# Performance work log

Hardware: AMD Instinct MI355X
Metric: run time of the kernel (lower is better)

## Reference

```python
import jax, jax.numpy as jnp
import numpy as np

B, S, D, DOM, L = 16, 512, 512, 8, 3  # batch, seq_len, mem_dim (S==D required by outputs*rel), domains, layers


def setup_inputs() -> dict:
    key = jax.random.key(0)
    ks = jax.random.split(key, 16)
    adj = jax.random.uniform(ks[0], (B, S, S), jnp.float32)
    rel = jax.random.uniform(ks[1], (B, S, S), jnp.float32)
    gcn_inputs = jax.random.normal(ks[2], (B, S, D), jnp.float32)
    frontrel = jax.random.normal(ks[3], (B, S, D), jnp.float32)
    backrel = jax.random.normal(ks[4], (B, S, D), jnp.float32)
    # depmap: exactly one selected column per (b, row) so masked_select reshapes to [B,S]
    depmap = jax.nn.one_hot(jax.random.randint(ks[5], (B, S), 0, S), S, dtype=jnp.float32)
    dom_idx = jax.random.randint(ks[6], (B, S), 0, DOM)
    has_dom = jax.random.bernoulli(ks[7], 0.5, (B, S)).astype(jnp.float32)
    domain_id = jax.nn.one_hot(dom_idx, DOM, dtype=jnp.float32) * has_dom[..., None]
    redom_idx = jax.random.randint(ks[8], (B, S), 0, DOM)
    has_re = jax.random.bernoulli(ks[9], 0.5, (B, S)).astype(jnp.float32)
    redomain_id = jax.nn.one_hot(redom_idx, DOM, dtype=jnp.float32) * has_re[..., None]
    domain = jax.random.bernoulli(ks[10], 0.5, (B, S, DOM, 1))
    mask = jnp.ones((B, S), dtype=bool)
    sc = 1.0 / np.sqrt(D)
    W_layers = jax.random.normal(ks[11], (L, D, D), jnp.float32) * sc
    b_layers = jnp.zeros((L, D), jnp.float32)
    prelu_a = jnp.full((L,), 0.25, jnp.float32)  # nn.PReLU default
    W_dg = jax.random.normal(ks[12], (D, D), jnp.float32) * sc
    b_dg = jnp.zeros((D,), jnp.float32)
    W_mg = jax.random.normal(ks[13], (2 * D, D), jnp.float32) * (1.0 / np.sqrt(2 * D))
    b_mg = jnp.zeros((D,), jnp.float32)
    W_out = jax.random.normal(ks[14], (L * D, D), jnp.float32) * (1.0 / np.sqrt(L * D))
    b_out = jnp.zeros((D,), jnp.float32)
    return dict(adj=adj, domain=domain, domain_id=domain_id, redomain_id=redomain_id,
                frontrel=frontrel, backrel=backrel, depmap=depmap, rel=rel,
                gcn_inputs=gcn_inputs, mask=mask, W_layers=W_layers, b_layers=b_layers,
                prelu_a=prelu_a, W_dg=W_dg, b_dg=b_dg, W_mg=W_mg, b_mg=b_mg,
                W_out=W_out, b_out=b_out)


def _forward(adj, domain, domain_id, redomain_id, frontrel, backrel, depmap, rel,
             gcn_inputs, W_layers, b_layers, prelu_a, W_dg, b_dg, W_mg, b_mg, W_out, b_out):
    denom = jnp.sum(adj, axis=2, keepdims=True) + 1.0                     # [B,S,1]
    domain_mask = jnp.sum(domain_id, axis=-1, keepdims=True) == 1.0       # [B,S,1]
    redomain_mask = jnp.sum(redomain_id, axis=-1, keepdims=True) == 1.0   # [B,S,1]
    frontadj = jnp.sum(adj * depmap, axis=-1)                             # [B,S]
    backadj = jnp.sum(jnp.swapaxes(adj, -1, -2) * depmap, axis=-1)        # [B,S]
    outputs = gcn_inputs
    outs = []
    for l in range(L):
        frontoutputs = jnp.where(domain_mask, 0.0, outputs)
        backoutputs = jnp.where(redomain_mask, 0.0, jnp.einsum('bij,bjd->bid', rel, outputs))
        # domain pooling: mask then max over sequence -> [B,DOM,D]
        pooled = jnp.max(jnp.where(domain, -10000.0, outputs[:, :, None, :]), axis=1)
        domain_outputs = jax.nn.sigmoid(pooled @ W_dg + b_dg)             # domain_gate
        frontoutputs = frontoutputs + jnp.einsum('bsk,bkd->bsd', domain_id, domain_outputs)
        backoutputs = backoutputs + jnp.einsum('bsk,bkd->bsd', redomain_id, domain_outputs)
        frontdepadj = jax.nn.sigmoid(jnp.concatenate([frontoutputs, frontrel], -1) @ W_mg + b_mg)
        backdepadj = jax.nn.sigmoid(jnp.concatenate([backoutputs, backrel], -1) @ W_mg + b_mg)
        delta = jnp.einsum('bji,bjd->bid', rel, frontadj[..., None] * frontdepadj * frontoutputs)
        delta = delta + backadj[..., None] * backdepadj * backoutputs
        Ax = jnp.einsum('bij,bjd->bid', adj, outputs * rel)               # requires S==D
        AxW = (Ax @ W_layers[l] + b_layers[l]) + (outputs @ W_layers[l] + b_layers[l]) + delta
        x = AxW / denom
        outputs = jnp.where(x >= 0, x, prelu_a[l] * x)                    # PReLU
        outs.append(outputs)                                              # dropout is eval-mode identity
    gcn_outputs = jnp.concatenate(outs, axis=2)                           # [B,S,L*D]
    return gcn_outputs @ W_out + b_out + gcn_inputs


def reference(adj, domain, domain_id, redomain_id, frontrel, backrel, depmap, rel,
              gcn_inputs, mask, W_layers, b_layers, prelu_a, W_dg, b_dg, W_mg, b_mg,
              W_out, b_out):
    return _forward(adj, domain, domain_id, redomain_id, frontrel, backrel, depmap, rel,
                    gcn_inputs, W_layers, b_layers, prelu_a, W_dg, b_dg, W_mg, b_mg,
                    W_out, b_out)
```

## Files before the change

### kernel.cpp

```cpp
#include <hip/hip_runtime.h>
#include <math.h>

#define SD_  (512*512)
#define BSD_ (16*512*512)

typedef unsigned short u16;
typedef short s16x8 __attribute__((ext_vector_type(8)));
typedef float f32x4 __attribute__((ext_vector_type(4)));

__device__ __forceinline__ float sigmoidf_(float x) { return 1.0f / (1.0f + __expf(-x)); }

__device__ __forceinline__ u16 f2bf(float f) {
    unsigned int u = __float_as_uint(f);
    u += 0x7fffu + ((u >> 16) & 1u);
    return (u16)(u >> 16);
}
__device__ __forceinline__ float bf2f(u16 h) { return __uint_as_float((unsigned)h << 16); }

__device__ __forceinline__ void glds16(const void* g, void* l) {
    __builtin_amdgcn_global_load_lds((const __attribute__((address_space(1))) unsigned int*)g,
                                     (__attribute__((address_space(3))) unsigned int*)l, 16, 0, 0);
}

struct GP {
    const u16 *A1, *A2;  int lda1, lda2;  long sA;
    const u16 *B1, *B2;  int ldb1, ldb2;  long sB;
    void *C1, *C2;  int obf1, obf2, ldc1, ldc2;  long sC;
    u16 *CT1, *CT2;  long sCT;
    const void *Ci1, *Ci2;  int cm1, cm2, ldci1, ldci2;  long sCi1, sCi2;
    const float *bias;  float bS;
    const float *sc1, *sc2;
    const int *selm1, *seli1, *selm2, *seli2;
    const float *DG;
    const float *invden, *prelu;  int pidx;
    int M, K, zs, swzX, swzY;
};

template<int EPI, int ASEL>
__global__ __launch_bounds__(512, 4)
void gemm3(const GP p)
{
    __shared__ short LS[32768];
    const int tid = threadIdx.x;
    int bx, by, bz;
    if (p.swzX >= 0) {
        const int bid = blockIdx.x + gridDim.x * (blockIdx.y + gridDim.y * blockIdx.z);
        const int ppx = (gridDim.y * gridDim.z) >> 3;
        const int xcd = bid & 7, idx = bid >> 3;
        const int pair = xcd * ppx + (idx >> p.swzX);
        bx = idx & ((1 << p.swzX) - 1);
        by = pair & ((1 << p.swzY) - 1);
        bz = pair >> p.swzY;
    } else { bx = blockIdx.x; by = blockIdx.y; bz = blockIdx.z; }

    const int seg = (bz >= p.zs) ? 1 : 0;
    const int z = seg ? bz - p.zs : bz;
    const u16* Ab = (seg ? p.A2 : p.A1) + z * p.sA;
    const int lda = seg ? p.lda2 : p.lda1;
    const u16* Bb = (seg ? p.B2 : p.B1) + z * p.sB;
    const int ldb = seg ? p.ldb2 : p.ldb1;

    const int m0 = by * 128, n0 = bx * 128;
    const int srow = ((tid >> 6) << 4) | (tid & 15);
    const int sk0 = ((tid >> 4) & 3) << 3;

    const u16* aRow = Ab + (long)(m0 + srow) * lda + sk0;
    const u16* bRow = Bb + (long)(n0 + srow) * ldb + sk0;

    int aselv = 0; long dgo = 0;
    if (ASEL) {
        const int* selm = seg ? p.selm2 : p.selm1;
        const int* seli = seg ? p.seli2 : p.seli1;
        const int r0 = m0 + srow;
        aselv = selm[r0];
        dgo = (long)(((r0 >> 9) << 3) + seli[r0]) * 512 + sk0;
    }

    auto stage = [&](int kk, int buf) {
        short* base = &LS[buf * 8192];
        if (ASEL) {
            s16x8 v;
            if (aselv) {
                const float* dg = p.DG + dgo + kk;
#pragma unroll
                for (int q = 0; q < 8; ++q) v[q] = (short)f2bf(dg[q]);
            } else v = *(const s16x8*)(aRow + kk);
            *(s16x8*)&base[tid * 8] = v;
        } else {
            glds16(aRow + kk, &base[tid * 8]);
        }
        glds16(bRow + kk, &base[4096 + tid * 8]);
    };

    const int wave = tid >> 6, lane = tid & 63;
    const int gA = (wave >> 2) << 2;
    const int gB = (wave & 3) << 1;

    f32x4 acc[4][2] = {};
    const int nkb = p.K >> 5;
    stage(0, 0);
    stage(32, 1);
    for (int kb = 0; kb < nkb; ++kb) {
        if (kb + 2 < nkb) stage((kb + 2) << 5, (kb + 2) & 3);
        const int ahead = (nkb - 1 - kb) < 2 ? (nkb - 1 - kb) : 2;
        if (ASEL) {
            if (ahead == 2)      asm volatile("s_waitcnt vmcnt(2)" ::: "memory");
            else if (ahead == 1) asm volatile("s_waitcnt vmcnt(1)" ::: "memory");
            else                 asm volatile("s_waitcnt vmcnt(0)" ::: "memory");
            asm volatile("s_waitcnt lgkmcnt(0)" ::: "memory");
        } else {
            if (ahead == 2)      asm volatile("s_waitcnt vmcnt(4)" ::: "memory");
            else if (ahead == 1) asm volatile("s_waitcnt vmcnt(2)" ::: "memory");
            else                 asm volatile("s_waitcnt vmcnt(0)" ::: "memory");
        }
        __builtin_amdgcn_s_barrier();
        const short* ls = &LS[(kb & 3) * 8192];
        s16x8 aF[4], bF[2];
#pragma unroll
        for (int mt = 0; mt < 4; ++mt) aF[mt] = *(const s16x8*)&ls[((gA + mt) * 64 + lane) * 8];
#pragma unroll
        for (int nt = 0; nt < 2; ++nt) bF[nt] = *(const s16x8*)&ls[4096 + ((gB + nt) * 64 + lane) * 8];
#pragma unroll
        for (int mt = 0; mt < 4; ++mt)
#pragma unroll
            for (int nt = 0; nt < 2; ++nt)
                acc[mt][nt] = __builtin_amdgcn_mfma_f32_16x16x32_bf16(aF[mt], bF[nt], acc[mt][nt], 0, 0, 0);
    }

    const int ml = lane & 15, quad = lane >> 4;
    const int wm = (wave >> 2) * 64, wn = (wave & 3) * 32;
    u16* Cb16 = (u16*)(seg ? p.C2 : p.C1);
    float* Cb32 = (float*)(seg ? p.C2 : p.C1);
    const int haveC = (seg ? p.C2 : p.C1) != nullptr;
    const int obf = seg ? p.obf2 : p.obf1;
    const int ldc = seg ? p.ldc2 : p.ldc1;
    if (haveC) { if (obf) Cb16 += z * p.sC; else Cb32 += z * p.sC; }
    u16* CTb = seg ? p.CT2 : p.CT1;
    if (CTb) CTb += z * p.sCT;
    const u16* CiT = (const u16*)(seg ? p.Ci2 : p.Ci1);
    const float* Ci32 = (const float*)(seg ? p.Ci2 : p.Ci1);
    const int cm = seg ? p.cm2 : p.cm1;
    const int ldci = seg ? p.ldci2 : p.ldci1;
    {
        const long sCi = seg ? p.sCi2 : p.sCi1;
        if (cm) CiT += z * sCi; else Ci32 += z * sCi;
    }
    const float pal = (EPI == 4) ? p.prelu[p.pidx] : 0.0f;
    const float* scp = (EPI == 8) ? (seg ? p.sc2 : p.sc1) : nullptr;
    const int* eselm = (EPI == 8) ? (seg ? p.selm2 : p.selm1) : nullptr;
    const int* eseli = (EPI == 8) ? (seg ? p.selm2 ? (seg ? p.seli2 : p.seli1) : p.seli1 : p.seli1) : nullptr;
    const int* eseli2 = (EPI == 8) ? (seg ? p.seli2 : p.seli1) : nullptr;

    const bool useEp = haveC && (obf == 1);
    u16* epbuf = (u16*)LS;
    if (useEp) __syncthreads();

#pragma unroll
    for (int mt = 0; mt < 4; ++mt) {
#pragma unroll
        for (int nt = 0; nt < 2; ++nt) {
            const int col = n0 + wn + nt * 16 + ml;
            const int rowb = m0 + wm + mt * 16 + quad * 4;
            float cin4[4];
            if (EPI == 3 || EPI == 4 || EPI == 7 || EPI == 8) {
                if (cm) {
                    const ushort4 c4 = *(const ushort4*)&CiT[(long)(rowb >> 9) * SD_ + (long)col * 512 + (rowb & 511)];
                    cin4[0] = bf2f(c4.x); cin4[1] = bf2f(c4.y); cin4[2] = bf2f(c4.z); cin4[3] = bf2f(c4.w);
                } else {
#pragma unroll
                    for (int r = 0; r < 4; ++r) cin4[r] = Ci32[(long)(rowb + r) * ldci + col];
                }
            }
            u16 pk[4];
#pragma unroll
            for (int r = 0; r < 4; ++r) {
                const int row = rowb + r;
                float x = acc[mt][nt][r];
                if (EPI == 1) x += p.bias[col];
                else if (EPI == 3) x += cin4[r];
                else if (EPI == 4) {
                    x = (x + p.bS * p.bias[col] + cin4[r]) * p.invden[z * p.M + row];
                    x = (x >= 0.0f) ? x : pal * x;
                }
                else if (EPI == 6) x = sigmoidf_(x + p.bias[col]);
                else if (EPI == 7) x += p.bias[col] + cin4[r];
                else if (EPI == 8) {
                    float av;
                    if (eselm[row]) av = p.DG[(long)(((row >> 9) << 3) + eseli2[row]) * 512 + col];
                    else av = bf2f(Ab[(long)row * lda + col]);
                    x = sigmoidf_(x + cin4[r]) * scp[row] * av;
                }
                if (haveC && obf == 0) Cb32[(long)row * ldc + col] = x;
                pk[r] = f2bf(x);
                if (useEp) epbuf[(wm + mt * 16 + quad * 4 + r) * 136 + wn + nt * 16 + ml] = pk[r];
            }
            if (CTb) {
                u16* ct = CTb + (long)(rowb >> 9) * SD_ + (long)col * 512 + (rowb & 511);
                *(ushort4*)ct = *(ushort4*)pk;
            }
        }
    }
    if (useEp) {
        __syncthreads();
        const int lr = tid >> 2, cs = (tid & 3) * 32;
#pragma unroll
        for (int j = 0; j < 4; ++j) {
            const s16x8 v = *(const s16x8*)&epbuf[lr * 136 + cs + j * 8];
            *(s16x8*)&Cb16[(long)(m0 + lr) * ldc + n0 + cs + j * 8] = v;
        }
    }
}

__global__ __launch_bounds__(256)
void cvt_k(const float* __restrict__ s, u16* __restrict__ d)
{
    const long i = ((long)blockIdx.x * 256 + threadIdx.x) * 4;
    const float4 v = *(const float4*)&s[i];
    ushort4 h = { f2bf(v.x), f2bf(v.y), f2bf(v.z), f2bf(v.w) };
    *(ushort4*)&d[i] = h;
}

__global__ __launch_bounds__(256)
void trcvt_k(const float* __restrict__ src, u16* __restrict__ dstT, u16* __restrict__ dstN,
             const int R, const int C, const long sS, const long sDT, const long sDN)
{
    __shared__ u16 t[64][72];
    const float* s = src + blockIdx.z * sS;
    const int r0 = blockIdx.y * 64, c0 = blockIdx.x * 64;
    const int tid = threadIdx.x;
    const int lr = tid >> 2, lc4 = (tid & 3) * 16;
#pragma unroll
    for (int j = 0; j < 4; ++j) {
        const float4 v = *(const float4*)&s[(long)(r0 + lr) * C + c0 + lc4 + j * 4];
        ushort4 h = { f2bf(v.x), f2bf(v.y), f2bf(v.z), f2bf(v.w) };
        *(ushort4*)&t[lr][lc4 + j * 4] = h;
        if (dstN) *(ushort4*)&dstN[blockIdx.z * sDN + (long)(r0 + lr) * C + c0 + lc4 + j * 4] = h;
    }
    __syncthreads();
    const int lcol = tid >> 2, rc = (tid & 3) * 16;
#pragma unroll
    for (int j = 0; j < 2; ++j) {
        s16x8 v;
#pragma unroll
        for (int q = 0; q < 8; ++q) v[q] = (short)t[rc + j * 8 + q][lcol];
        *(s16x8*)&dstT[blockIdx.z * sDT + (long)(c0 + lcol) * R + r0 + rc + j * 8] = v;
    }
}

__global__ __launch_bounds__(256)
void e0_k(const float* __restrict__ adj, const float* __restrict__ depmap,
          const float* __restrict__ domain_id, const float* __restrict__ redomain_id,
          float* __restrict__ invden, float* __restrict__ fa, int* __restrict__ dcol,
          int* __restrict__ dm, int* __restrict__ dsel, int* __restrict__ rm, int* __restrict__ rsel)
{
    const int bs = blockIdx.x;
    const int t = threadIdx.x;
    const float* arow = adj + (long)bs * 512;
    const float* drow = depmap + (long)bs * 512;
    __shared__ float red[256];
    __shared__ int scol;
    if (t == 0) scol = 0;
    const float a0 = arow[t], a1 = arow[t + 256];
    const float p0 = drow[t], p1 = drow[t + 256];
    if (p0 > 0.5f) scol = t;
    if (p1 > 0.5f) scol = t + 256;
    red[t] = a0 + a1;
    __syncthreads();
    for (int off = 128; off > 0; off >>= 1) { if (t < off) red[t] += red[t + off]; __syncthreads(); }
    if (t == 0) invden[bs] = 1.0f / (red[0] + 1.0f);
    __syncthreads();
    red[t] = a0 * p0 + a1 * p1;
    __syncthreads();
    for (int off = 128; off > 0; off >>= 1) { if (t < off) red[t] += red[t + off]; __syncthreads(); }
    if (t == 0) {
        fa[bs] = red[0];
        dcol[bs] = scol;
        const float* q = domain_id + (long)bs * 8;
        float s = 0.f; int sel = 0;
        for (int k = 0; k < 8; ++k) { float v = q[k]; s += v; if (v > 0.5f) sel = k; }
        dm[bs] = (s > 0.5f) ? 1 : 0; dsel[bs] = sel;
        const float* r = redomain_id + (long)bs * 8;
        s = 0.f; sel = 0;
        for (int k = 0; k < 8; ++k) { float v = r[k]; s += v; if (v > 0.5f) sel = k; }
        rm[bs] = (s > 0.5f) ? 1 : 0; rsel[bs] = sel;
    }
}

__global__ void e0b_k(const float* __restrict__ adj, const int* __restrict__ dcol, float* __restrict__ ba)
{
    const int bs = blockIdx.x * 256 + threadIdx.x;
    const int b = bs >> 9, s = bs & 511;
    ba[bs] = adj[((long)b * 512 + dcol[bs]) * 512 + s];
}

__global__ __launch_bounds__(256)
void pool1_k(const u16* __restrict__ OUT, const int ldO, const int* __restrict__ domain,
             const u16* __restrict__ relb, u16* __restrict__ cm, u16* __restrict__ OxRT)
{
    const int b = blockIdx.x >> 4, c = blockIdx.x & 15;
    const int s0 = c * 32, tid = threadIdx.x;
    __shared__ int dom[256];
    dom[tid] = domain[((long)(b * 512 + s0 + (tid >> 3))) * 8 + (tid & 7)];
    __syncthreads();
    const int d0 = tid * 2;
    float mxa[8], mxb[8];
#pragma unroll
    for (int k = 0; k < 8; ++k) { mxa[k] = -10000.0f; mxb[k] = -10000.0f; }
    s16x8 pA[4], pB[4];
#pragma unroll
    for (int s = 0; s < 32; ++s) {
        const int row = b * 512 + s0 + s;
        const unsigned uv = *(const unsigned*)&OUT[(long)row * ldO + d0];
        const unsigned rv = *(const unsigned*)&relb[(long)row * 512 + d0];
        const float vx = bf2f((u16)(uv & 0xffff)), vy = bf2f((u16)(uv >> 16));
        const float rx = bf2f((u16)(rv & 0xffff)), ry = bf2f((u16)(rv >> 16));
        pA[s >> 3][s & 7] = (short)f2bf(vx * rx);
        pB[s >> 3][s & 7] = (short)f2bf(vy * ry);
        const int* ds = &dom[s * 8];
#pragma unroll
        for (int k = 0; k < 8; ++k) {
            mxa[k] = fmaxf(mxa[k], ds[k] ? -10000.0f : vx);
            mxb[k] = fmaxf(mxb[k], ds[k] ? -10000.0f : vy);
        }
    }
#pragma unroll
    for (int j = 0; j < 4; ++j) *(s16x8*)&OxRT[((long)b * 512 + d0) * 512 + s0 + j * 8] = pA[j];
#pragma unroll
    for (int j = 0; j < 4; ++j) *(s16x8*)&OxRT[((long)b * 512 + d0 + 1) * 512 + s0 + j * 8] = pB[j];
#pragma unroll
    for (int k = 0; k < 8; ++k) {
        ushort2 h = { f2bf(mxa[k]), f2bf(mxb[k]) };
        *(ushort2*)&cm[((long)((b * 16 + c) * 8 + k)) * 512 + d0] = h;
    }
}

__global__ void pool2_k(const u16* __restrict__ cm, u16* __restrict__ pooled)
{
    const int q = blockIdx.x * 256 + threadIdx.x;
    const int b = q >> 12, k = (q >> 9) & 7, d = q & 511;
    float m = -1e30f;
    for (int c = 0; c < 16; ++c)
        m = fmaxf(m, bf2f(cm[((long)((b * 16 + c) * 8 + k)) * 512 + d]));
    pooled[((long)(b * 8 + k)) * 512 + d] = f2bf(m);
}

extern "C" void kernel_launch(void* const* d_in, const int* in_sizes, int n_in,
                              void* d_out, int out_size, void* d_ws, size_t ws_size,
                              hipStream_t stream)
{
    const float* adj         = (const float*)d_in[0];
    const int*   domain      = (const int*)d_in[1];
    const float* domain_id   = (const float*)d_in[2];
    const float* redomain_id = (const float*)d_in[3];
    const float* frontrel    = (const float*)d_in[4];
    const float* backrel     = (const float*)d_in[5];
    const float* depmap      = (const float*)d_in[6];
    const float* rel         = (const float*)d_in[7];
    const float* gcn         = (const float*)d_in[8];
    const float* W_layers    = (const float*)d_in[10];
    const float* b_layers    = (const float*)d_in[11];
    const float* prelu_a     = (const float*)d_in[12];
    const float* W_dg        = (const float*)d_in[13];
    const float* b_dg        = (const float*)d_in[14];
    const float* W_mg        = (const float*)d_in[15];
    const float* b_mg        = (const float*)d_in[16];
    const float* W_out       = (const float*)d_in[17];
    const float* b_out       = (const float*)d_in[18];
    float* out = (float*)d_out;

    char* w = (char*)d_ws;
    auto alloc = [&](size_t bytes) { void* p = (void*)w; w += (bytes + 255) & ~(size_t)255; return p; };
    const size_t Bb = (size_t)BSD_ * 2;
    u16* OUTS_bf = (u16*)alloc((size_t)8192 * 1536 * 2);
    u16* OUTT    = (u16*)alloc(Bb);
    u16* gcnT    = (u16*)alloc(Bb);
    u16* RB_bf   = (u16*)alloc(Bb);
    u16* XBT     = (u16*)alloc(Bb);
    u16* XFT     = (u16*)alloc(Bb);
    u16* OxRT    = (u16*)alloc(Bb);
    u16* DLT     = (u16*)alloc(Bb);
    u16* AXO_bf  = (u16*)alloc(Bb);
    u16* BBT     = (u16*)alloc(Bb);
    u16* FBT     = (u16*)alloc(Bb);
    u16* rel_bf  = (u16*)alloc(Bb);
    u16* relT_bf = (u16*)alloc(Bb);
    u16* adj_bf  = (u16*)alloc(Bb);
    u16* gcn_bf  = (u16*)alloc(Bb);
    u16* frel_bf = (u16*)alloc(Bb);
    u16* brel_bf = (u16*)alloc(Bb);
    u16* WmgT1 = (u16*)alloc((size_t)SD_ * 2);
    u16* WmgT2 = (u16*)alloc((size_t)SD_ * 2);
    u16* WdgT  = (u16*)alloc((size_t)SD_ * 2);
    u16* WlT   = (u16*)alloc((size_t)3 * SD_ * 2);
    u16* WoutT = (u16*)alloc((size_t)512 * 1536 * 2);
    u16* cm     = (u16*)alloc((size_t)16 * 16 * 8 * 512 * 2);
    u16* pooled = (u16*)alloc((size_t)16 * 8 * 512 * 2);
    float* DG     = (float*)alloc((size_t)16 * 8 * 512 * 4);
    float* invden = (float*)alloc(8192 * 4);
    float* fa     = (float*)alloc(8192 * 4);
    float* ba     = (float*)alloc(8192 * 4);
    int* dcol = (int*)alloc(8192 * 4);
    int* dm   = (int*)alloc(8192 * 4);
    int* dsel = (int*)alloc(8192 * 4);
    int* rm   = (int*)alloc(8192 * 4);
    int* rsel = (int*)alloc(8192 * 4);

    cvt_k<<<4096, 256, 0, stream>>>(adj, adj_bf);
    cvt_k<<<4096, 256, 0, stream>>>(frontrel, frel_bf);
    cvt_k<<<4096, 256, 0, stream>>>(backrel, brel_bf);
    trcvt_k<<<dim3(8, 8, 16), 256, 0, stream>>>(gcn, gcnT, gcn_bf, 512, 512, SD_, SD_, SD_);
    trcvt_k<<<dim3(8, 8, 16), 256, 0, stream>>>(rel, relT_bf, rel_bf, 512, 512, SD_, SD_, SD_);
    trcvt_k<<<dim3(8, 8, 1), 256, 0, stream>>>(W_mg, WmgT1, nullptr, 512, 512, 0, 0, 0);
    trcvt_k<<<dim3(8, 8, 1), 256, 0, stream>>>(W_mg + SD_, WmgT2, nullptr, 512, 512, 0, 0, 0);
    trcvt_k<<<dim3(8, 8, 1), 256, 0, stream>>>(W_dg, WdgT, nullptr, 512, 512, 0, 0, 0);
    trcvt_k<<<dim3(8, 8, 3), 256, 0, stream>>>(W_layers, WlT, nullptr, 512, 512, SD_, SD_, 0);
    trcvt_k<<<dim3(8, 24, 1), 256, 0, stream>>>(W_out, WoutT, nullptr, 1536, 512, 0, 0, 0);
    e0_k<<<8192, 256, 0, stream>>>(adj, depmap, domain_id, redomain_id, invden, fa, dcol, dm, dsel, rm, rsel);
    e0b_k<<<32, 256, 0, stream>>>(adj, dcol, ba);

    const dim3 blk(512);

    {
        GP p{};
        p.A1 = brel_bf; p.A2 = frel_bf; p.lda1 = p.lda2 = 512; p.sA = 0;
        p.B1 = p.B2 = WmgT2; p.ldb1 = p.ldb2 = 512; p.sB = 0;
        p.CT1 = BBT; p.CT2 = FBT; p.sCT = 0;
        p.bias = b_mg; p.M = 8192; p.K = 512; p.zs = 1; p.swzX = 2; p.swzY = 6;
        gemm3<1, 0><<<dim3(4, 64, 2), blk, 0, stream>>>(p);
    }

    for (int l = 0; l < 3; ++l) {
        const u16* OUTp  = (l == 0) ? gcn_bf : (OUTS_bf + (l - 1) * 512);
        const u16* OUTTp = (l == 0) ? gcnT : OUTT;
        const int ldO = (l == 0) ? 512 : 1536;

        {
            GP p{};
            p.A1 = rel_bf; p.lda1 = 512; p.sA = SD_;
            p.B1 = OUTTp; p.ldb1 = 512; p.sB = SD_;
            p.C1 = RB_bf; p.obf1 = 1; p.ldc1 = 512; p.sC = SD_;
            p.M = 512; p.K = 512; p.zs = 16; p.swzX = 2; p.swzY = 2;
            gemm3<0, 0><<<dim3(4, 4, 16), blk, 0, stream>>>(p);
        }
        pool1_k<<<256, 256, 0, stream>>>(OUTp, ldO, domain, rel_bf, cm, OxRT);
        pool2_k<<<256, 256, 0, stream>>>(cm, pooled);
        {
            GP p{};
            p.A1 = pooled; p.lda1 = 512; p.B1 = WdgT; p.ldb1 = 512;
            p.C1 = DG; p.obf1 = 0; p.ldc1 = 512;
            p.bias = b_dg; p.M = 128; p.K = 512; p.zs = 1; p.swzX = -1;
            gemm3<6, 0><<<dim3(4, 1, 1), blk, 0, stream>>>(p);
        }
        {
            GP p{};
            p.A1 = RB_bf; p.lda1 = 512; p.A2 = OUTp; p.lda2 = ldO; p.sA = 0;
            p.selm1 = rm; p.seli1 = rsel; p.selm2 = dm; p.seli2 = dsel; p.DG = DG;
            p.B1 = p.B2 = WmgT1; p.ldb1 = p.ldb2 = 512; p.sB = 0;
            p.Ci1 = BBT; p.Ci2 = FBT; p.cm1 = p.cm2 = 1; p.ldci1 = p.ldci2 = 512; p.sCi1 = p.sCi2 = 0;
            p.CT1 = XBT; p.CT2 = XFT; p.sCT = 0;
            p.sc1 = ba; p.sc2 = fa; p.M = 8192; p.K = 512; p.zs = 1; p.swzX = 2; p.swzY = 6;
            gemm3<8, 1><<<dim3(4, 64, 2), blk, 0, stream>>>(p);
        }
        {
            GP p{};
            p.A1 = relT_bf; p.lda1 = 512; p.A2 = adj_bf; p.lda2 = 512; p.sA = SD_;
            p.B1 = XFT; p.ldb1 = 512;
            p.B2 = OxRT; p.ldb2 = 512; p.sB = SD_;
            p.Ci1 = XBT; p.cm1 = 1; p.ldci1 = 512; p.sCi1 = SD_;
            p.Ci2 = OUTTp; p.cm2 = 1; p.ldci2 = 512; p.sCi2 = SD_;
            p.CT1 = DLT; p.sCT = SD_;
            p.C2 = AXO_bf; p.obf2 = 1; p.ldc2 = 512; p.sC = SD_;
            p.M = 512; p.K = 512; p.zs = 16; p.swzX = 2; p.swzY = 2;
            gemm3<3, 0><<<dim3(4, 4, 32), blk, 0, stream>>>(p);
        }
        {
            GP p{};
            p.A1 = AXO_bf; p.lda1 = 512; p.sA = SD_;
            p.B1 = WlT + (long)l * SD_; p.ldb1 = 512; p.sB = 0;
            p.Ci1 = DLT; p.cm1 = 1; p.ldci1 = 512; p.sCi1 = SD_;
            p.C1 = OUTS_bf + l * 512; p.obf1 = 1; p.ldc1 = 1536; p.sC = (long)512 * 1536;
            p.CT1 = OUTT; p.sCT = SD_;
            p.bias = b_layers + l * 512; p.bS = 2.0f;
            p.invden = invden; p.prelu = prelu_a; p.pidx = l;
            p.M = 512; p.K = 512; p.zs = 16; p.swzX = 2; p.swzY = 2;
            gemm3<4, 0><<<dim3(4, 4, 16), blk, 0, stream>>>(p);
        }
    }

    {
        GP p{};
        p.A1 = OUTS_bf; p.lda1 = 1536; p.sA = 0;
        p.B1 = WoutT; p.ldb1 = 1536; p.sB = 0;
        p.Ci1 = gcn; p.cm1 = 0; p.ldci1 = 512; p.sCi1 = 0;
        p.C1 = out; p.obf1 = 0; p.ldc1 = 512; p.sC = 0;
        p.bias = b_out; p.M = 8192; p.K = 1536; p.zs = 1; p.swzX = 2; p.swzY = 6;
        gemm3<7, 0><<<dim3(4, 64, 1), blk, 0, stream>>>(p);
    }
}
```

Before: 756.7 us.

## Use BK=64 double-buffered async LDS staging and bf16 DG for selected rows

The GEMM main loop now stages 64-wide K tiles into two LDS buffers and issues four global_load_lds per tile, replacing the previous triple-buffered 32-wide scheme. The DG gate matrix is now written and read as bf16. This lets ASEL rows also use async direct-to-LDS loads by redirecting the row pointer, instead of register loads that convert fp32 to bf16. The aim is fewer barriers and waitcnt stalls per K and no per-element conversion in staging, at the cost of an extra barrier per iteration, a shallower prefetch depth and rounding DG to bf16 in the epilogue.

```diff
diff --git a/kernel.cpp b/kernel.cpp
--- a/kernel.cpp
+++ b/kernel.cpp
@@ -31,7 +31,7 @@
     const float *bias;  float bS;
     const float *sc1, *sc2;
     const int *selm1, *seli1, *selm2, *seli2;
-    const float *DG;
+    const u16 *DG;
     const float *invden, *prelu;  int pidx;
     int M, K, zs, swzX, swzY;
 };
@@ -63,33 +63,24 @@
     const int m0 = by * 128, n0 = bx * 128;
     const int srow = ((tid >> 6) << 4) | (tid & 15);
     const int sk0 = ((tid >> 4) & 3) << 3;
+    const int slot = ((srow >> 4) << 9) + (sk0 << 4) + ((srow & 15) << 3);
 
     const u16* aRow = Ab + (long)(m0 + srow) * lda + sk0;
-    const u16* bRow = Bb + (long)(n0 + srow) * ldb + sk0;
-
-    int aselv = 0; long dgo = 0;
     if (ASEL) {
         const int* selm = seg ? p.selm2 : p.selm1;
         const int* seli = seg ? p.seli2 : p.seli1;
         const int r0 = m0 + srow;
-        aselv = selm[r0];
-        dgo = (long)(((r0 >> 9) << 3) + seli[r0]) * 512 + sk0;
-    }
-
-    auto stage = [&](int kk, int buf) {
-        short* base = &LS[buf * 8192];
-        if (ASEL) {
-            s16x8 v;
-            if (aselv) {
-                const float* dg = p.DG + dgo + kk;
-#pragma unroll
-                for (int q = 0; q < 8; ++q) v[q] = (short)f2bf(dg[q]);
-            } else v = *(const s16x8*)(aRow + kk);
-            *(s16x8*)&base[tid * 8] = v;
-        } else {
-            glds16(aRow + kk, &base[tid * 8]);
-        }
-        glds16(bRow + kk, &base[4096 + tid * 8]);
+        if (selm[r0]) aRow = p.DG + (long)(((r0 >> 9) << 3) + seli[r0]) * 512 + sk0;
+    }
+    const u16* bRow = Bb + (long)(n0 + srow) * ldb + sk0;
+
+    auto stage = [&](int kb2) {
+        short* base = &LS[(kb2 & 1) * 16384];
+        const int kk = kb2 << 6;
+        glds16(aRow + kk,      &base[slot]);
+        glds16(aRow + kk + 32, &base[4096 + slot]);
+        glds16(bRow + kk,      &base[8192 + slot]);
+        glds16(bRow + kk + 32, &base[12288 + slot]);
     };
 
     const int wave = tid >> 6, lane = tid & 63;
@@ -97,34 +88,32 @@
     const int gB = (wave & 3) << 1;
 
     f32x4 acc[4][2] = {};
-    const int nkb = p.K >> 5;
-    stage(0, 0);
-    stage(32, 1);
+    const int nkb = p.K >> 6;
+
+    stage(0);
     for (int kb = 0; kb < nkb; ++kb) {
-        if (kb + 2 < nkb) stage((kb + 2) << 5, (kb + 2) & 3);
-        const int ahead = (nkb - 1 - kb) < 2 ? (nkb - 1 - kb) : 2;
-        if (ASEL) {
-            if (ahead == 2)      asm volatile("s_waitcnt vmcnt(2)" ::: "memory");
-            else if (ahead == 1) asm volatile("s_waitcnt vmcnt(1)" ::: "memory");
-            else                 asm volatile("s_waitcnt vmcnt(0)" ::: "memory");
-            asm volatile("s_waitcnt lgkmcnt(0)" ::: "memory");
+        if (kb + 1 < nkb) {
+            stage(kb + 1);
+            asm volatile("s_waitcnt vmcnt(4)" ::: "memory");
         } else {
-            if (ahead == 2)      asm volatile("s_waitcnt vmcnt(4)" ::: "memory");
-            else if (ahead == 1) asm volatile("s_waitcnt vmcnt(2)" ::: "memory");
-            else                 asm volatile("s_waitcnt vmcnt(0)" ::: "memory");
+            asm volatile("s_waitcnt vmcnt(0)" ::: "memory");
         }
         __builtin_amdgcn_s_barrier();
-        const short* ls = &LS[(kb & 3) * 8192];
-        s16x8 aF[4], bF[2];
-#pragma unroll
-        for (int mt = 0; mt < 4; ++mt) aF[mt] = *(const s16x8*)&ls[((gA + mt) * 64 + lane) * 8];
-#pragma unroll
-        for (int nt = 0; nt < 2; ++nt) bF[nt] = *(const s16x8*)&ls[4096 + ((gB + nt) * 64 + lane) * 8];
-#pragma unroll
-        for (int mt = 0; mt < 4; ++mt)
-#pragma unroll
-            for (int nt = 0; nt < 2; ++nt)
-                acc[mt][nt] = __builtin_amdgcn_mfma_f32_16x16x32_bf16(aF[mt], bF[nt], acc[mt][nt], 0, 0, 0);
+        const short* ls = &LS[(kb & 1) * 16384];
+#pragma unroll
+        for (int kh = 0; kh < 2; ++kh) {
+            s16x8 aF[4], bF[2];
+#pragma unroll
+            for (int mt = 0; mt < 4; ++mt) aF[mt] = *(const s16x8*)&ls[kh * 4096 + ((gA + mt) * 64 + lane) * 8];
+#pragma unroll
+            for (int nt = 0; nt < 2; ++nt) bF[nt] = *(const s16x8*)&ls[8192 + kh * 4096 + ((gB + nt) * 64 + lane) * 8];
+#pragma unroll
+            for (int mt = 0; mt < 4; ++mt)
+#pragma unroll
+                for (int nt = 0; nt < 2; ++nt)
+                    acc[mt][nt] = __builtin_amdgcn_mfma_f32_16x16x32_bf16(aF[mt], bF[nt], acc[mt][nt], 0, 0, 0);
+        }
+        __builtin_amdgcn_s_barrier();
     }
 
     const int ml = lane & 15, quad = lane >> 4;
@@ -148,7 +137,6 @@
     const float pal = (EPI == 4) ? p.prelu[p.pidx] : 0.0f;
     const float* scp = (EPI == 8) ? (seg ? p.sc2 : p.sc1) : nullptr;
     const int* eselm = (EPI == 8) ? (seg ? p.selm2 : p.selm1) : nullptr;
-    const int* eseli = (EPI == 8) ? (seg ? p.selm2 ? (seg ? p.seli2 : p.seli1) : p.seli1 : p.seli1) : nullptr;
     const int* eseli2 = (EPI == 8) ? (seg ? p.seli2 : p.seli1) : nullptr;
 
     const bool useEp = haveC && (obf == 1);
@@ -186,7 +174,7 @@
                 else if (EPI == 7) x += p.bias[col] + cin4[r];
                 else if (EPI == 8) {
                     float av;
-                    if (eselm[row]) av = p.DG[(long)(((row >> 9) << 3) + eseli2[row]) * 512 + col];
+                    if (eselm[row]) av = bf2f(p.DG[(long)(((row >> 9) << 3) + eseli2[row]) * 512 + col]);
                     else av = bf2f(Ab[(long)row * lda + col]);
                     x = sigmoidf_(x + cin4[r]) * scp[row] * av;
                 }
@@ -395,7 +383,7 @@
     u16* WoutT = (u16*)alloc((size_t)512 * 1536 * 2);
     u16* cm     = (u16*)alloc((size_t)16 * 16 * 8 * 512 * 2);
     u16* pooled = (u16*)alloc((size_t)16 * 8 * 512 * 2);
-    float* DG     = (float*)alloc((size_t)16 * 8 * 512 * 4);
+    u16* DGb    = (u16*)alloc((size_t)16 * 8 * 512 * 2);
     float* invden = (float*)alloc(8192 * 4);
     float* fa     = (float*)alloc(8192 * 4);
     float* ba     = (float*)alloc(8192 * 4);
@@ -447,14 +435,14 @@
         {
             GP p{};
             p.A1 = pooled; p.lda1 = 512; p.B1 = WdgT; p.ldb1 = 512;
-            p.C1 = DG; p.obf1 = 0; p.ldc1 = 512;
+            p.C1 = DGb; p.obf1 = 1; p.ldc1 = 512;
             p.bias = b_dg; p.M = 128; p.K = 512; p.zs = 1; p.swzX = -1;
             gemm3<6, 0><<<dim3(4, 1, 1), blk, 0, stream>>>(p);
         }
         {
             GP p{};
             p.A1 = RB_bf; p.lda1 = 512; p.A2 = OUTp; p.lda2 = ldO; p.sA = 0;
-            p.selm1 = rm; p.seli1 = rsel; p.selm2 = dm; p.seli2 = dsel; p.DG = DG;
+            p.selm1 = rm; p.seli1 = rsel; p.selm2 = dm; p.seli2 = dsel; p.DG = DGb;
             p.B1 = p.B2 = WmgT1; p.ldb1 = p.ldb2 = 512; p.sB = 0;
             p.Ci1 = BBT; p.Ci2 = FBT; p.cm1 = p.cm2 = 1; p.ldci1 = p.ldci2 = 512; p.sCi1 = p.sCi2 = 0;
             p.CT1 = XBT; p.CT2 = XFT; p.sCT = 0;
```

New measurement: 682.8 us. 1.11x faster.
